# Kernel optimization log

Measured on AMD Instinct MI355X. Metric: run time of the kernel, lower is better.

## Reference

```python
import jax, jax.numpy as jnp
import numpy as np

N, IN_DIM, L, K, D = 131072, 128, 16, 8, 50
ENC_H, DEC_H, HEAD_H, DF = 64, 16, 64, 1.0


def setup_inputs() -> dict:
    key = jax.random.key(0)
    ks = jax.random.split(key, 20)
    s = lambda k, shape, fan: jax.random.normal(k, shape, jnp.float32) * (1.0 / np.sqrt(fan))
    return {
        "x": jax.random.normal(ks[0], (N, IN_DIM), jnp.float32),
        # encoder: in -> 64 -> 64 -> L
        "We1": s(ks[1], (IN_DIM, ENC_H), IN_DIM), "be1": jnp.zeros((ENC_H,), jnp.float32),
        "We2": s(ks[2], (ENC_H, ENC_H), ENC_H),   "be2": jnp.zeros((ENC_H,), jnp.float32),
        "We3": s(ks[3], (ENC_H, L), ENC_H),       "be3": jnp.zeros((L,), jnp.float32),
        # decoder: L -> 16 -> in
        "Wd1": s(ks[4], (L, DEC_H), L),           "bd1": jnp.zeros((DEC_H,), jnp.float32),
        "Wd2": s(ks[5], (DEC_H, IN_DIM), DEC_H),  "bd2": jnp.zeros((IN_DIM,), jnp.float32),
        # K per-cluster survival heads: (L+in) -> 64 -> num_durations
        "Wh1": s(ks[6], (K, L + IN_DIM, HEAD_H), L + IN_DIM), "bh1": jnp.zeros((K, HEAD_H), jnp.float32),
        "Wh2": s(ks[7], (K, HEAD_H, D), HEAD_H),              "bh2": jnp.zeros((K, D), jnp.float32),
        # cluster centers buffer
        "centers": jax.random.normal(ks[8], (K, L), jnp.float32) * 0.05,
    }


def _student_t_sim(z, centers, df):
    # z: [N, L], centers: [K, L] -> q: [N, K]
    dist2 = jnp.sum((z[:, None, :] - centers[None, :, :]) ** 2, axis=-1)
    logits = -0.5 * (df + 1.0) * jnp.log1p(dist2 / df)
    return jax.nn.softmax(logits, axis=1)


def reference(x, We1, be1, We2, be2, We3, be3, Wd1, bd1, Wd2, bd2,
              Wh1, bh1, Wh2, bh2, centers):
    relu = jax.nn.relu
    # encoder (eval mode: dropout off, non-variational)
    e = relu(x @ We1 + be1)
    e = relu(e @ We2 + be2)
    z = e @ We3 + be3                      # [N, L]
    q = _student_t_sim(z, centers, DF)     # [N, K]
    h = jnp.concatenate([z, x], axis=1)    # [N, L+in]
    # cluster-argmax routing to per-cluster heads: compute all K, select winner
    cluster_idx = jnp.argmax(q, axis=1)    # [N]
    h1 = relu(jnp.einsum("nf,kfh->nkh", h, Wh1) + bh1[None])   # [N, K, H]
    lg = jnp.einsum("nkh,khd->nkd", h1, Wh2) + bh2[None]       # [N, K, D]
    surv_logits = jnp.take_along_axis(lg, cluster_idx[:, None, None], axis=1)[:, 0]  # [N, D]
    # decoder + reconstruction loss per sample
    d = relu(z @ Wd1 + bd1)
    x_hat = d @ Wd2 + bd2                  # [N, in]
    rec_ps = jnp.mean((x_hat - x) ** 2, axis=1)
    kld = jnp.zeros((x.shape[0],), x.dtype)
    return z, q, surv_logits, x_hat, rec_ps, kld
```

## Files before the change

### kernel.cpp

```cpp
#include <hip/hip_runtime.h>

#define NS 131072
#define INDIM 128
#define LDIM 16
#define KC 8
#define DD 50
#define EH 64
#define DH 16
#define HH 64

typedef unsigned long long u64;

__global__ __launch_bounds__(256) void k_enc(
    const float* __restrict__ x,
    const float* __restrict__ We1, const float* __restrict__ be1,
    const float* __restrict__ We2, const float* __restrict__ be2,
    const float* __restrict__ We3, const float* __restrict__ be3,
    const float* __restrict__ Wd1, const float* __restrict__ bd1,
    const float* __restrict__ Wd2, const float* __restrict__ bd2,
    const float* __restrict__ centers,
    float* __restrict__ out,
    int* __restrict__ cidx, int* __restrict__ counts)
{
    const int t = threadIdx.x;
    const int s = blockIdx.x * 256 + t;
    __shared__ float buf[16][257];

    const float4* x4 = reinterpret_cast<const float4*>(x + (size_t)s * INDIM);

    float a1[EH];
    #pragma unroll
    for (int j = 0; j < EH; ++j) a1[j] = be1[j];
    for (int fc = 0; fc < INDIM / 4; ++fc) {
        float4 v = x4[fc];
        float xr[4] = {v.x, v.y, v.z, v.w};
        #pragma unroll
        for (int fl = 0; fl < 4; ++fl) {
            const float* w = We1 + (fc * 4 + fl) * EH;
            #pragma unroll
            for (int j = 0; j < EH; ++j) a1[j] = fmaf(xr[fl], w[j], a1[j]);
        }
    }
    #pragma unroll
    for (int j = 0; j < EH; ++j) a1[j] = fmaxf(a1[j], 0.0f);

    float a2[EH];
    #pragma unroll
    for (int j = 0; j < EH; ++j) a2[j] = be2[j];
    for (int hc = 0; hc < 4; ++hc) {
        #pragma unroll
        for (int hl = 0; hl < 16; ++hl) buf[hl][t] = a1[hc * 16 + hl];
        __syncthreads();
        for (int hl = 0; hl < 16; ++hl) {
            float ev = buf[hl][t];
            const float* w = We2 + (hc * 16 + hl) * EH;
            #pragma unroll
            for (int j = 0; j < EH; ++j) a2[j] = fmaf(ev, w[j], a2[j]);
        }
        __syncthreads();
    }
    #pragma unroll
    for (int j = 0; j < EH; ++j) a2[j] = fmaxf(a2[j], 0.0f);

    float z[LDIM];
    #pragma unroll
    for (int j = 0; j < LDIM; ++j) z[j] = be3[j];
    for (int hc = 0; hc < 4; ++hc) {
        #pragma unroll
        for (int hl = 0; hl < 16; ++hl) buf[hl][t] = a2[hc * 16 + hl];
        __syncthreads();
        for (int hl = 0; hl < 16; ++hl) {
            float ev = buf[hl][t];
            const float* w = We3 + (hc * 16 + hl) * LDIM;
            #pragma unroll
            for (int j = 0; j < LDIM; ++j) z[j] = fmaf(ev, w[j], z[j]);
        }
        __syncthreads();
    }

    {
        float4* oz = reinterpret_cast<float4*>(out + (size_t)s * LDIM);
        oz[0] = make_float4(z[0], z[1], z[2], z[3]);
        oz[1] = make_float4(z[4], z[5], z[6], z[7]);
        oz[2] = make_float4(z[8], z[9], z[10], z[11]);
        oz[3] = make_float4(z[12], z[13], z[14], z[15]);
    }

    float d2[KC];
    #pragma unroll
    for (int k = 0; k < KC; ++k) {
        float acc = 0.0f;
        #pragma unroll
        for (int l = 0; l < LDIM; ++l) {
            float dl = z[l] - centers[k * LDIM + l];
            acc = fmaf(dl, dl, acc);
        }
        d2[k] = acc;
    }
    float lgt[KC];
    #pragma unroll
    for (int k = 0; k < KC; ++k) lgt[k] = -log1pf(d2[k]);
    float m = lgt[0];
    #pragma unroll
    for (int k = 1; k < KC; ++k) m = fmaxf(m, lgt[k]);
    float ex[KC];
    float ssum = 0.0f;
    #pragma unroll
    for (int k = 0; k < KC; ++k) { ex[k] = expf(lgt[k] - m); ssum += ex[k]; }
    {
        float q[KC];
        #pragma unroll
        for (int k = 0; k < KC; ++k) q[k] = ex[k] / ssum;
        float4* oq = reinterpret_cast<float4*>(out + (size_t)NS * LDIM + (size_t)s * KC);
        oq[0] = make_float4(q[0], q[1], q[2], q[3]);
        oq[1] = make_float4(q[4], q[5], q[6], q[7]);
    }
    int ci = 0;
    float best = d2[0];
    #pragma unroll
    for (int k = 1; k < KC; ++k) if (d2[k] < best) { best = d2[k]; ci = k; }
    cidx[s] = ci;

    #pragma unroll
    for (int k = 0; k < KC; ++k) {
        u64 mk = __ballot(ci == k);
        if ((t & 63) == 0 && mk) atomicAdd(&counts[k], (int)__popcll(mk));
    }

    float dh[DH];
    #pragma unroll
    for (int j = 0; j < DH; ++j) dh[j] = bd1[j];
    #pragma unroll
    for (int h = 0; h < LDIM; ++h) {
        float zv = z[h];
        #pragma unroll
        for (int j = 0; j < DH; ++j) dh[j] = fmaf(zv, Wd1[h * DH + j], dh[j]);
    }
    #pragma unroll
    for (int j = 0; j < DH; ++j) dh[j] = fmaxf(dh[j], 0.0f);

    float rec = 0.0f;
    float* oxh = out + (size_t)NS * 74 + (size_t)s * INDIM;
    for (int jc = 0; jc < 8; ++jc) {
        float xh[16];
        #pragma unroll
        for (int j = 0; j < 16; ++j) xh[j] = bd2[jc * 16 + j];
        #pragma unroll
        for (int h = 0; h < DH; ++h) {
            float dv = dh[h];
            #pragma unroll
            for (int j = 0; j < 16; ++j)
                xh[j] = fmaf(dv, Wd2[h * INDIM + jc * 16 + j], xh[j]);
        }
        float4 xa = x4[jc * 4 + 0], xb = x4[jc * 4 + 1];
        float4 xc = x4[jc * 4 + 2], xd = x4[jc * 4 + 3];
        float xs[16] = {xa.x, xa.y, xa.z, xa.w, xb.x, xb.y, xb.z, xb.w,
                        xc.x, xc.y, xc.z, xc.w, xd.x, xd.y, xd.z, xd.w};
        #pragma unroll
        for (int j = 0; j < 16; ++j) {
            float df_ = xh[j] - xs[j];
            rec = fmaf(df_, df_, rec);
        }
        float4* o4 = reinterpret_cast<float4*>(oxh + jc * 16);
        o4[0] = make_float4(xh[0], xh[1], xh[2], xh[3]);
        o4[1] = make_float4(xh[4], xh[5], xh[6], xh[7]);
        o4[2] = make_float4(xh[8], xh[9], xh[10], xh[11]);
        o4[3] = make_float4(xh[12], xh[13], xh[14], xh[15]);
    }
    out[(size_t)NS * 202 + s] = rec * (1.0f / 128.0f);
    out[(size_t)NS * 203 + s] = 0.0f;
}

__global__ void k_scan(const int* __restrict__ counts,
                       int* __restrict__ bases, int* __restrict__ cursors)
{
    if (threadIdx.x == 0) {
        int acc = 0;
        for (int k = 0; k < KC; ++k) {
            bases[k] = acc;
            cursors[k] = acc;
            acc += counts[k];
        }
    }
}

__global__ __launch_bounds__(256) void k_scatter(
    const int* __restrict__ cidx, int* __restrict__ cursors, int* __restrict__ seg)
{
    const int s = blockIdx.x * 256 + threadIdx.x;
    const int lane = threadIdx.x & 63;
    const int ci = cidx[s];
    #pragma unroll
    for (int k = 0; k < KC; ++k) {
        u64 mk = __ballot(ci == k);
        if (ci == k) {
            const int leader = __ffsll(mk) - 1;
            int base = 0;
            if (lane == leader) base = atomicAdd(&cursors[k], (int)__popcll(mk));
            base = __shfl(base, leader, 64);
            const int pos = base + (int)__popcll(mk & (((u64)1 << lane) - 1));
            seg[pos] = s;
        }
    }
}

__global__ __launch_bounds__(256) void k_heads(
    const float* __restrict__ x, const float* __restrict__ zread,
    const float* __restrict__ Wh1, const float* __restrict__ bh1,
    const float* __restrict__ Wh2, const float* __restrict__ bh2,
    const int* __restrict__ counts, const int* __restrict__ bases,
    const int* __restrict__ seg,
    float* __restrict__ surv)
{
    __shared__ float buf[16][257];
    const int b = blockIdx.x;
    int k = -1, chunk = 0, pref = 0;
    #pragma unroll
    for (int kk = 0; kk < KC; ++kk) {
        int ck = (counts[kk] + 255) >> 8;
        if (k < 0) {
            if (b < pref + ck) { k = kk; chunk = b - pref; }
            pref += ck;
        }
    }
    if (k < 0) return;
    const int cnt = counts[k];
    const int t = threadIdx.x;
    const int i = chunk * 256 + t;
    const bool act = i < cnt;
    const int idx = act ? seg[bases[k] + i] : 0;

    float a[HH];
    #pragma unroll
    for (int j = 0; j < HH; ++j) a[j] = bh1[k * HH + j];

    const float4* z4 = reinterpret_cast<const float4*>(zread + (size_t)idx * LDIM);
    for (int fc = 0; fc < 4; ++fc) {
        float4 v = z4[fc];
        float r[4] = {v.x, v.y, v.z, v.w};
        #pragma unroll
        for (int fl = 0; fl < 4; ++fl) {
            const float* w = Wh1 + ((size_t)k * 144 + fc * 4 + fl) * HH;
            #pragma unroll
            for (int j = 0; j < HH; ++j) a[j] = fmaf(r[fl], w[j], a[j]);
        }
    }
    const float4* xx4 = reinterpret_cast<const float4*>(x + (size_t)idx * INDIM);
    for (int fc = 0; fc < 32; ++fc) {
        float4 v = xx4[fc];
        float r[4] = {v.x, v.y, v.z, v.w};
        #pragma unroll
        for (int fl = 0; fl < 4; ++fl) {
            const float* w = Wh1 + ((size_t)k * 144 + 16 + fc * 4 + fl) * HH;
            #pragma unroll
            for (int j = 0; j < HH; ++j) a[j] = fmaf(r[fl], w[j], a[j]);
        }
    }
    #pragma unroll
    for (int j = 0; j < HH; ++j) a[j] = fmaxf(a[j], 0.0f);

    float lg[DD];
    #pragma unroll
    for (int j = 0; j < DD; ++j) lg[j] = bh2[k * DD + j];
    for (int hc = 0; hc < 4; ++hc) {
        #pragma unroll
        for (int hl = 0; hl < 16; ++hl) buf[hl][t] = a[hc * 16 + hl];
        __syncthreads();
        for (int hl = 0; hl < 16; ++hl) {
            float hv = buf[hl][t];
            const float* w = Wh2 + ((size_t)k * HH + hc * 16 + hl) * DD;
            #pragma unroll
            for (int j = 0; j < DD; ++j) lg[j] = fmaf(hv, w[j], lg[j]);
        }
        __syncthreads();
    }
    if (act) {
        float2* srow = reinterpret_cast<float2*>(surv + (size_t)idx * DD);
        #pragma unroll
        for (int j = 0; j < DD / 2; ++j) srow[j] = make_float2(lg[2 * j], lg[2 * j + 1]);
    }
}

extern "C" void kernel_launch(void* const* d_in, const int* in_sizes, int n_in,
                              void* d_out, int out_size, void* d_ws, size_t ws_size,
                              hipStream_t stream)
{
    const float* x   = (const float*)d_in[0];
    const float* We1 = (const float*)d_in[1];
    const float* be1 = (const float*)d_in[2];
    const float* We2 = (const float*)d_in[3];
    const float* be2 = (const float*)d_in[4];
    const float* We3 = (const float*)d_in[5];
    const float* be3 = (const float*)d_in[6];
    const float* Wd1 = (const float*)d_in[7];
    const float* bd1 = (const float*)d_in[8];
    const float* Wd2 = (const float*)d_in[9];
    const float* bd2 = (const float*)d_in[10];
    const float* Wh1 = (const float*)d_in[11];
    const float* bh1 = (const float*)d_in[12];
    const float* Wh2 = (const float*)d_in[13];
    const float* bh2 = (const float*)d_in[14];
    const float* cen = (const float*)d_in[15];
    float* out = (float*)d_out;

    int* cidx    = (int*)d_ws;
    int* counts  = cidx + NS;
    int* bases   = counts + KC;
    int* cursors = bases + KC;
    int* seg     = cursors + KC;

    hipMemsetAsync(counts, 0, KC * sizeof(int), stream);

    k_enc<<<dim3(NS / 256), dim3(256), 0, stream>>>(
        x, We1, be1, We2, be2, We3, be3, Wd1, bd1, Wd2, bd2, cen,
        out, cidx, counts);

    k_scan<<<dim3(1), dim3(64), 0, stream>>>(counts, bases, cursors);

    k_scatter<<<dim3(NS / 256), dim3(256), 0, stream>>>(cidx, cursors, seg);

    k_heads<<<dim3(NS / 256 + KC), dim3(256), 0, stream>>>(
        x, out , Wh1, bh1, Wh2, bh2,
        counts, bases, seg, out + (size_t)NS * 24 );
}
```

Measured before the change: 524.5 us.

## Split each sample across four threads and move decoder into heads kernel

Both the encoder and the heads kernel now give each sample to four threads, each owning a quarter of the output features. The sample's x (and z) row is staged through padded shared memory with coalesced loads, replacing per-thread strided row reads, and per-thread register arrays shrink from 64 to 16 accumulators, which should raise occupancy. The decoder and reconstruction loss move into the heads kernel so the gathered x row is reused there. The cost is more blocks, more barriers, and weight loads repeated across the four thread groups.

```diff
diff --git a/kernel.cpp b/kernel.cpp
--- a/kernel.cpp
+++ b/kernel.cpp
@@ -1,13 +1,7 @@
 #include <hip/hip_runtime.h>
 
 #define NS 131072
-#define INDIM 128
-#define LDIM 16
 #define KC 8
-#define DD 50
-#define EH 64
-#define DH 16
-#define HH 64
 
 typedef unsigned long long u64;
 
@@ -16,159 +10,117 @@
     const float* __restrict__ We1, const float* __restrict__ be1,
     const float* __restrict__ We2, const float* __restrict__ be2,
     const float* __restrict__ We3, const float* __restrict__ be3,
-    const float* __restrict__ Wd1, const float* __restrict__ bd1,
-    const float* __restrict__ Wd2, const float* __restrict__ bd2,
     const float* __restrict__ centers,
-    float* __restrict__ out,
+    float* __restrict__ out_z, float* __restrict__ out_q,
     int* __restrict__ cidx, int* __restrict__ counts)
 {
-    const int t = threadIdx.x;
-    const int s = blockIdx.x * 256 + t;
-    __shared__ float buf[16][257];
-
-    const float4* x4 = reinterpret_cast<const float4*>(x + (size_t)s * INDIM);
-
-    float a1[EH];
-    #pragma unroll
-    for (int j = 0; j < EH; ++j) a1[j] = be1[j];
-    for (int fc = 0; fc < INDIM / 4; ++fc) {
-        float4 v = x4[fc];
-        float xr[4] = {v.x, v.y, v.z, v.w};
-        #pragma unroll
-        for (int fl = 0; fl < 4; ++fl) {
-            const float* w = We1 + (fc * 4 + fl) * EH;
+    __shared__ float sm[64*129 + 64*17];
+    float* xs = sm;
+    float* zs = sm + 64*129;
+
+    const int t  = threadIdx.x;
+    const int s  = t & 63;
+    const int qw = t >> 6;
+    const int s0 = blockIdx.x * 64;
+
+    {
+        const float4* xg = reinterpret_cast<const float4*>(x + (size_t)s0 * 128);
+        #pragma unroll
+        for (int c = 0; c < 8; ++c) {
+            int i = t + c * 256;
+            float4 v = xg[i];
+            float* p = xs + (i >> 5) * 129 + (i & 31) * 4;
+            p[0] = v.x; p[1] = v.y; p[2] = v.z; p[3] = v.w;
+        }
+    }
+    __syncthreads();
+
+    float a[16];
+    #pragma unroll
+    for (int j = 0; j < 16; ++j) a[j] = be1[qw*16 + j];
+    #pragma unroll 4
+    for (int f = 0; f < 128; ++f) {
+        float xv = xs[s*129 + f];
+        const float* w = We1 + f*64 + qw*16;
+        #pragma unroll
+        for (int j = 0; j < 16; ++j) a[j] = fmaf(xv, w[j], a[j]);
+    }
+    #pragma unroll
+    for (int j = 0; j < 16; ++j) a[j] = fmaxf(a[j], 0.f);
+    __syncthreads();
+    #pragma unroll
+    for (int j = 0; j < 16; ++j) xs[s*65 + qw*16 + j] = a[j];
+    __syncthreads();
+
+    float b[16];
+    #pragma unroll
+    for (int j = 0; j < 16; ++j) b[j] = be2[qw*16 + j];
+    #pragma unroll 4
+    for (int f = 0; f < 64; ++f) {
+        float ev = xs[s*65 + f];
+        const float* w = We2 + f*64 + qw*16;
+        #pragma unroll
+        for (int j = 0; j < 16; ++j) b[j] = fmaf(ev, w[j], b[j]);
+    }
+    #pragma unroll
+    for (int j = 0; j < 16; ++j) b[j] = fmaxf(b[j], 0.f);
+    __syncthreads();
+    #pragma unroll
+    for (int j = 0; j < 16; ++j) xs[s*65 + qw*16 + j] = b[j];
+    __syncthreads();
+
+    float z4[4];
+    #pragma unroll
+    for (int j = 0; j < 4; ++j) z4[j] = be3[qw*4 + j];
+    #pragma unroll 4
+    for (int f = 0; f < 64; ++f) {
+        float ev = xs[s*65 + f];
+        const float* w = We3 + f*16 + qw*4;
+        #pragma unroll
+        for (int j = 0; j < 4; ++j) z4[j] = fmaf(ev, w[j], z4[j]);
+    }
+    #pragma unroll
+    for (int j = 0; j < 4; ++j) zs[s*17 + qw*4 + j] = z4[j];
+    *reinterpret_cast<float4*>(out_z + (size_t)(s0 + s)*16 + qw*4) =
+        make_float4(z4[0], z4[1], z4[2], z4[3]);
+    __syncthreads();
+
+    if (qw == 0) {
+        float zz[16];
+        #pragma unroll
+        for (int l = 0; l < 16; ++l) zz[l] = zs[s*17 + l];
+        float d2[KC];
+        #pragma unroll
+        for (int k = 0; k < KC; ++k) {
+            float acc = 0.f;
             #pragma unroll
-            for (int j = 0; j < EH; ++j) a1[j] = fmaf(xr[fl], w[j], a1[j]);
-        }
-    }
-    #pragma unroll
-    for (int j = 0; j < EH; ++j) a1[j] = fmaxf(a1[j], 0.0f);
-
-    float a2[EH];
-    #pragma unroll
-    for (int j = 0; j < EH; ++j) a2[j] = be2[j];
-    for (int hc = 0; hc < 4; ++hc) {
-        #pragma unroll
-        for (int hl = 0; hl < 16; ++hl) buf[hl][t] = a1[hc * 16 + hl];
-        __syncthreads();
-        for (int hl = 0; hl < 16; ++hl) {
-            float ev = buf[hl][t];
-            const float* w = We2 + (hc * 16 + hl) * EH;
-            #pragma unroll
-            for (int j = 0; j < EH; ++j) a2[j] = fmaf(ev, w[j], a2[j]);
-        }
-        __syncthreads();
-    }
-    #pragma unroll
-    for (int j = 0; j < EH; ++j) a2[j] = fmaxf(a2[j], 0.0f);
-
-    float z[LDIM];
-    #pragma unroll
-    for (int j = 0; j < LDIM; ++j) z[j] = be3[j];
-    for (int hc = 0; hc < 4; ++hc) {
-        #pragma unroll
-        for (int hl = 0; hl < 16; ++hl) buf[hl][t] = a2[hc * 16 + hl];
-        __syncthreads();
-        for (int hl = 0; hl < 16; ++hl) {
-            float ev = buf[hl][t];
-            const float* w = We3 + (hc * 16 + hl) * LDIM;
-            #pragma unroll
-            for (int j = 0; j < LDIM; ++j) z[j] = fmaf(ev, w[j], z[j]);
-        }
-        __syncthreads();
-    }
-
-    {
-        float4* oz = reinterpret_cast<float4*>(out + (size_t)s * LDIM);
-        oz[0] = make_float4(z[0], z[1], z[2], z[3]);
-        oz[1] = make_float4(z[4], z[5], z[6], z[7]);
-        oz[2] = make_float4(z[8], z[9], z[10], z[11]);
-        oz[3] = make_float4(z[12], z[13], z[14], z[15]);
-    }
-
-    float d2[KC];
-    #pragma unroll
-    for (int k = 0; k < KC; ++k) {
-        float acc = 0.0f;
-        #pragma unroll
-        for (int l = 0; l < LDIM; ++l) {
-            float dl = z[l] - centers[k * LDIM + l];
-            acc = fmaf(dl, dl, acc);
-        }
-        d2[k] = acc;
-    }
-    float lgt[KC];
-    #pragma unroll
-    for (int k = 0; k < KC; ++k) lgt[k] = -log1pf(d2[k]);
-    float m = lgt[0];
-    #pragma unroll
-    for (int k = 1; k < KC; ++k) m = fmaxf(m, lgt[k]);
-    float ex[KC];
-    float ssum = 0.0f;
-    #pragma unroll
-    for (int k = 0; k < KC; ++k) { ex[k] = expf(lgt[k] - m); ssum += ex[k]; }
-    {
-        float q[KC];
-        #pragma unroll
-        for (int k = 0; k < KC; ++k) q[k] = ex[k] / ssum;
-        float4* oq = reinterpret_cast<float4*>(out + (size_t)NS * LDIM + (size_t)s * KC);
-        oq[0] = make_float4(q[0], q[1], q[2], q[3]);
-        oq[1] = make_float4(q[4], q[5], q[6], q[7]);
-    }
-    int ci = 0;
-    float best = d2[0];
-    #pragma unroll
-    for (int k = 1; k < KC; ++k) if (d2[k] < best) { best = d2[k]; ci = k; }
-    cidx[s] = ci;
-
-    #pragma unroll
-    for (int k = 0; k < KC; ++k) {
-        u64 mk = __ballot(ci == k);
-        if ((t & 63) == 0 && mk) atomicAdd(&counts[k], (int)__popcll(mk));
-    }
-
-    float dh[DH];
-    #pragma unroll
-    for (int j = 0; j < DH; ++j) dh[j] = bd1[j];
-    #pragma unroll
-    for (int h = 0; h < LDIM; ++h) {
-        float zv = z[h];
-        #pragma unroll
-        for (int j = 0; j < DH; ++j) dh[j] = fmaf(zv, Wd1[h * DH + j], dh[j]);
-    }
-    #pragma unroll
-    for (int j = 0; j < DH; ++j) dh[j] = fmaxf(dh[j], 0.0f);
-
-    float rec = 0.0f;
-    float* oxh = out + (size_t)NS * 74 + (size_t)s * INDIM;
-    for (int jc = 0; jc < 8; ++jc) {
-        float xh[16];
-        #pragma unroll
-        for (int j = 0; j < 16; ++j) xh[j] = bd2[jc * 16 + j];
-        #pragma unroll
-        for (int h = 0; h < DH; ++h) {
-            float dv = dh[h];
-            #pragma unroll
-            for (int j = 0; j < 16; ++j)
-                xh[j] = fmaf(dv, Wd2[h * INDIM + jc * 16 + j], xh[j]);
-        }
-        float4 xa = x4[jc * 4 + 0], xb = x4[jc * 4 + 1];
-        float4 xc = x4[jc * 4 + 2], xd = x4[jc * 4 + 3];
-        float xs[16] = {xa.x, xa.y, xa.z, xa.w, xb.x, xb.y, xb.z, xb.w,
-                        xc.x, xc.y, xc.z, xc.w, xd.x, xd.y, xd.z, xd.w};
-        #pragma unroll
-        for (int j = 0; j < 16; ++j) {
-            float df_ = xh[j] - xs[j];
-            rec = fmaf(df_, df_, rec);
-        }
-        float4* o4 = reinterpret_cast<float4*>(oxh + jc * 16);
-        o4[0] = make_float4(xh[0], xh[1], xh[2], xh[3]);
-        o4[1] = make_float4(xh[4], xh[5], xh[6], xh[7]);
-        o4[2] = make_float4(xh[8], xh[9], xh[10], xh[11]);
-        o4[3] = make_float4(xh[12], xh[13], xh[14], xh[15]);
-    }
-    out[(size_t)NS * 202 + s] = rec * (1.0f / 128.0f);
-    out[(size_t)NS * 203 + s] = 0.0f;
+            for (int l = 0; l < 16; ++l) {
+                float dl = zz[l] - centers[k*16 + l];
+                acc = fmaf(dl, dl, acc);
+            }
+            d2[k] = acc;
+        }
+        float lgt[KC], ex[KC];
+        float m = -1e30f;
+        #pragma unroll
+        for (int k = 0; k < KC; ++k) { lgt[k] = -log1pf(d2[k]); m = fmaxf(m, lgt[k]); }
+        float ssum = 0.f;
+        #pragma unroll
+        for (int k = 0; k < KC; ++k) { ex[k] = expf(lgt[k] - m); ssum += ex[k]; }
+        float inv = 1.f / ssum;
+        float4* oq = reinterpret_cast<float4*>(out_q + (size_t)(s0 + s)*8);
+        oq[0] = make_float4(ex[0]*inv, ex[1]*inv, ex[2]*inv, ex[3]*inv);
+        oq[1] = make_float4(ex[4]*inv, ex[5]*inv, ex[6]*inv, ex[7]*inv);
+        int ci = 0; float best = d2[0];
+        #pragma unroll
+        for (int k = 1; k < KC; ++k) if (d2[k] < best) { best = d2[k]; ci = k; }
+        cidx[s0 + s] = ci;
+        #pragma unroll
+        for (int k = 0; k < KC; ++k) {
+            u64 mk = __ballot(ci == k);
+            if (s == 0 && mk) atomicAdd(&counts[k], (int)__popcll(mk));
+        }
+    }
 }
 
 __global__ void k_scan(const int* __restrict__ counts,
@@ -206,78 +158,137 @@
 
 __global__ __launch_bounds__(256) void k_heads(
     const float* __restrict__ x, const float* __restrict__ zread,
+    const float* __restrict__ Wd1, const float* __restrict__ bd1,
+    const float* __restrict__ Wd2, const float* __restrict__ bd2,
     const float* __restrict__ Wh1, const float* __restrict__ bh1,
     const float* __restrict__ Wh2, const float* __restrict__ bh2,
     const int* __restrict__ counts, const int* __restrict__ bases,
     const int* __restrict__ seg,
-    float* __restrict__ surv)
-{
-    __shared__ float buf[16][257];
-    const int b = blockIdx.x;
+    float* __restrict__ surv, float* __restrict__ xhat,
+    float* __restrict__ rec, float* __restrict__ kld)
+{
+    __shared__ float sm[64*145 + 64*5];
+    __shared__ int idxs[64];
+    float* xz = sm;
+    float* rr = sm + 64*145;
+
+    const int bq = blockIdx.x;
     int k = -1, chunk = 0, pref = 0;
     #pragma unroll
     for (int kk = 0; kk < KC; ++kk) {
-        int ck = (counts[kk] + 255) >> 8;
+        int ck = (counts[kk] + 63) >> 6;
         if (k < 0) {
-            if (b < pref + ck) { k = kk; chunk = b - pref; }
+            if (bq < pref + ck) { k = kk; chunk = bq - pref; }
             pref += ck;
         }
     }
     if (k < 0) return;
     const int cnt = counts[k];
-    const int t = threadIdx.x;
-    const int i = chunk * 256 + t;
-    const bool act = i < cnt;
-    const int idx = act ? seg[bases[k] + i] : 0;
-
-    float a[HH];
-    #pragma unroll
-    for (int j = 0; j < HH; ++j) a[j] = bh1[k * HH + j];
-
-    const float4* z4 = reinterpret_cast<const float4*>(zread + (size_t)idx * LDIM);
-    for (int fc = 0; fc < 4; ++fc) {
-        float4 v = z4[fc];
-        float r[4] = {v.x, v.y, v.z, v.w};
-        #pragma unroll
-        for (int fl = 0; fl < 4; ++fl) {
-            const float* w = Wh1 + ((size_t)k * 144 + fc * 4 + fl) * HH;
-            #pragma unroll
-            for (int j = 0; j < HH; ++j) a[j] = fmaf(r[fl], w[j], a[j]);
-        }
-    }
-    const float4* xx4 = reinterpret_cast<const float4*>(x + (size_t)idx * INDIM);
-    for (int fc = 0; fc < 32; ++fc) {
-        float4 v = xx4[fc];
-        float r[4] = {v.x, v.y, v.z, v.w};
-        #pragma unroll
-        for (int fl = 0; fl < 4; ++fl) {
-            const float* w = Wh1 + ((size_t)k * 144 + 16 + fc * 4 + fl) * HH;
-            #pragma unroll
-            for (int j = 0; j < HH; ++j) a[j] = fmaf(r[fl], w[j], a[j]);
-        }
-    }
-    #pragma unroll
-    for (int j = 0; j < HH; ++j) a[j] = fmaxf(a[j], 0.0f);
-
-    float lg[DD];
-    #pragma unroll
-    for (int j = 0; j < DD; ++j) lg[j] = bh2[k * DD + j];
-    for (int hc = 0; hc < 4; ++hc) {
-        #pragma unroll
-        for (int hl = 0; hl < 16; ++hl) buf[hl][t] = a[hc * 16 + hl];
-        __syncthreads();
-        for (int hl = 0; hl < 16; ++hl) {
-            float hv = buf[hl][t];
-            const float* w = Wh2 + ((size_t)k * HH + hc * 16 + hl) * DD;
-            #pragma unroll
-            for (int j = 0; j < DD; ++j) lg[j] = fmaf(hv, w[j], lg[j]);
-        }
-        __syncthreads();
-    }
+    const int t  = threadIdx.x;
+    const int s  = t & 63;
+    const int qw = t >> 6;
+    const bool act = (chunk*64 + s) < cnt;
+
+    if (t < 64) {
+        int ii = chunk*64 + t;
+        idxs[t] = seg[bases[k] + ((ii < cnt) ? ii : 0)];
+    }
+    __syncthreads();
+
+    {
+        int row = t >> 2, c4 = t & 3;
+        float4 v = reinterpret_cast<const float4*>(zread + (size_t)idxs[row]*16)[c4];
+        float* p = xz + row*145 + c4*4;
+        p[0] = v.x; p[1] = v.y; p[2] = v.z; p[3] = v.w;
+    }
+    #pragma unroll
+    for (int c = 0; c < 8; ++c) {
+        int ii = t + c*256;
+        int row = ii >> 5, c4 = ii & 31;
+        float4 v = reinterpret_cast<const float4*>(x + (size_t)idxs[row]*128)[c4];
+        float* p = xz + row*145 + 16 + c4*4;
+        p[0] = v.x; p[1] = v.y; p[2] = v.z; p[3] = v.w;
+    }
+    __syncthreads();
+
+    const int idx = idxs[s];
+
+    float d[16];
+    #pragma unroll
+    for (int j = 0; j < 16; ++j) d[j] = bd1[j];
+    #pragma unroll
+    for (int h = 0; h < 16; ++h) {
+        float zv = xz[s*145 + h];
+        const float* w = Wd1 + h*16;
+        #pragma unroll
+        for (int j = 0; j < 16; ++j) d[j] = fmaf(zv, w[j], d[j]);
+    }
+    #pragma unroll
+    for (int j = 0; j < 16; ++j) d[j] = fmaxf(d[j], 0.f);
+
+    float xh[32];
+    #pragma unroll
+    for (int j = 0; j < 32; ++j) xh[j] = bd2[qw*32 + j];
+    #pragma unroll
+    for (int h = 0; h < 16; ++h) {
+        float dv = d[h];
+        const float* w = Wd2 + h*128 + qw*32;
+        #pragma unroll
+        for (int j = 0; j < 32; ++j) xh[j] = fmaf(dv, w[j], xh[j]);
+    }
+    float rp = 0.f;
+    #pragma unroll
+    for (int j = 0; j < 32; ++j) {
+        float df_ = xh[j] - xz[s*145 + 16 + qw*32 + j];
+        rp = fmaf(df_, df_, rp);
+    }
+    rr[s*5 + qw] = rp;
     if (act) {
-        float2* srow = reinterpret_cast<float2*>(surv + (size_t)idx * DD);
-        #pragma unroll
-        for (int j = 0; j < DD / 2; ++j) srow[j] = make_float2(lg[2 * j], lg[2 * j + 1]);
+        float4* o4 = reinterpret_cast<float4*>(xhat + (size_t)idx*128 + qw*32);
+        #pragma unroll
+        for (int j = 0; j < 8; ++j)
+            o4[j] = make_float4(xh[4*j], xh[4*j+1], xh[4*j+2], xh[4*j+3]);
+    }
+    __syncthreads();
+    if (qw == 0 && act) {
+        float rs = rr[s*5+0] + rr[s*5+1] + rr[s*5+2] + rr[s*5+3];
+        rec[idx] = rs * (1.0f/128.0f);
+        kld[idx] = 0.f;
+    }
+
+    float a[16];
+    #pragma unroll
+    for (int j = 0; j < 16; ++j) a[j] = bh1[k*64 + qw*16 + j];
+    #pragma unroll 4
+    for (int f = 0; f < 144; ++f) {
+        float hv = xz[s*145 + f];
+        const float* w = Wh1 + ((size_t)k*144 + f)*64 + qw*16;
+        #pragma unroll
+        for (int j = 0; j < 16; ++j) a[j] = fmaf(hv, w[j], a[j]);
+    }
+    #pragma unroll
+    for (int j = 0; j < 16; ++j) a[j] = fmaxf(a[j], 0.f);
+    __syncthreads();
+    #pragma unroll
+    for (int j = 0; j < 16; ++j) xz[s*65 + qw*16 + j] = a[j];
+    __syncthreads();
+
+    const int nd   = (qw < 2) ? 13 : 12;
+    const int base = (qw < 2) ? qw*13 : 26 + (qw - 2)*12;
+    float lg[13];
+    #pragma unroll
+    for (int j = 0; j < 13; ++j) lg[j] = bh2[k*50 + base + ((j < nd) ? j : 0)];
+    #pragma unroll 4
+    for (int h = 0; h < 64; ++h) {
+        float hv = xz[s*65 + h];
+        const float* w = Wh2 + ((size_t)k*64 + h)*50 + base;
+        #pragma unroll
+        for (int j = 0; j < 13; ++j) lg[j] = fmaf(hv, w[(j < nd) ? j : 0], lg[j]);
+    }
+    if (act) {
+        float* so = surv + (size_t)idx*50 + base;
+        #pragma unroll
+        for (int j = 0; j < 13; ++j) if (j < nd) so[j] = lg[j];
     }
 }
 
@@ -303,6 +314,13 @@
     const float* cen = (const float*)d_in[15];
     float* out = (float*)d_out;
 
+    float* out_z  = out;
+    float* out_q  = out + (size_t)NS * 16;
+    float* out_sv = out + (size_t)NS * 24;
+    float* out_xh = out + (size_t)NS * 74;
+    float* out_rc = out + (size_t)NS * 202;
+    float* out_kl = out + (size_t)NS * 203;
+
     int* cidx    = (int*)d_ws;
     int* counts  = cidx + NS;
     int* bases   = counts + KC;
@@ -311,15 +329,14 @@
 
     hipMemsetAsync(counts, 0, KC * sizeof(int), stream);
 
-    k_enc<<<dim3(NS / 256), dim3(256), 0, stream>>>(
-        x, We1, be1, We2, be2, We3, be3, Wd1, bd1, Wd2, bd2, cen,
-        out, cidx, counts);
+    k_enc<<<dim3(NS / 64), dim3(256), 0, stream>>>(
+        x, We1, be1, We2, be2, We3, be3, cen, out_z, out_q, cidx, counts);
 
     k_scan<<<dim3(1), dim3(64), 0, stream>>>(counts, bases, cursors);
 
     k_scatter<<<dim3(NS / 256), dim3(256), 0, stream>>>(cidx, cursors, seg);
 
-    k_heads<<<dim3(NS / 256 + KC), dim3(256), 0, stream>>>(
-        x, out , Wh1, bh1, Wh2, bh2,
-        counts, bases, seg, out + (size_t)NS * 24 );
-}
+    k_heads<<<dim3(NS / 64 + KC), dim3(256), 0, stream>>>(
+        x, out_z, Wd1, bd1, Wd2, bd2, Wh1, bh1, Wh2, bh2,
+        counts, bases, seg, out_sv, out_xh, out_rc, out_kl);
+}
```

Result: slower. 705.5 us (+34.5%).
